# Kernel optimization log

Hardware: AMD Instinct MI355X
Metric: run time of the kernel (lower is better)

Reference implementation:

```python
import jax, jax.numpy as jnp
import numpy as np

N_NODES = 100000
N_EDGES = 400000
N_GRAPHS = 4096
D = 300          # emb_dim
L = 5            # num_layers
NUM_ATOM, NUM_CHIR = 120, 3
NUM_BOND, NUM_DIR = 6, 3
SELF_LOOP_BOND = 4
TEMP = 0.04


def setup_inputs() -> dict:
    key = jax.random.key(0)
    ks = jax.random.split(key, 24)
    inp = {}
    # graph batch 0
    inp["x0"] = jax.random.randint(ks[0], (N_NODES, 2), 0, 3)
    inp["edge_index0"] = jax.random.randint(ks[1], (2, N_EDGES), 0, N_NODES)
    inp["edge_attr0"] = jax.random.randint(ks[2], (N_EDGES, 2), 0, 3)
    inp["batch_ids0"] = jnp.sort(jax.random.randint(ks[3], (N_NODES,), 0, N_GRAPHS))
    inp["dangling0"] = jax.random.randint(ks[4], (N_GRAPHS,), 0, N_NODES)
    # graph batch 1
    inp["x1"] = jax.random.randint(ks[5], (N_NODES, 2), 0, 3)
    inp["edge_index1"] = jax.random.randint(ks[6], (2, N_EDGES), 0, N_NODES)
    inp["edge_attr1"] = jax.random.randint(ks[7], (N_EDGES, 2), 0, 3)
    inp["batch_ids1"] = jnp.sort(jax.random.randint(ks[8], (N_NODES,), 0, N_GRAPHS))
    inp["dangling1"] = jax.random.randint(ks[9], (N_GRAPHS,), 0, N_NODES)
    # shared encoder parameters
    g = lambda i, shp, s=0.1: (jax.random.normal(ks[i], shp, jnp.float32) * s)
    inp["atom_emb1"] = g(10, (NUM_ATOM, D))
    inp["atom_emb2"] = g(11, (NUM_CHIR, D))
    inp["eemb1"] = g(12, (L, NUM_BOND, D))
    inp["eemb2"] = g(13, (L, NUM_DIR, D))
    inp["W1"] = g(14, (L, D, 2 * D))
    inp["b1"] = jnp.zeros((L, 2 * D), jnp.float32)
    inp["W2"] = g(15, (L, 2 * D, D))
    inp["b2"] = jnp.zeros((L, D), jnp.float32)
    inp["bn_g"] = jnp.ones((L, D), jnp.float32)
    inp["bn_b"] = jnp.zeros((L, D), jnp.float32)
    # projectors stacked: 0=projector0, 1=projector1, 2=dangling_proj0, 3=dangling_proj1
    inp["pW1"] = g(16, (4, D, D))
    inp["pb1"] = jnp.zeros((4, D), jnp.float32)
    inp["pW2"] = g(17, (4, D, D))
    inp["pb2"] = jnp.zeros((4, D), jnp.float32)
    return inp


def _encode(x, edge_index, edge_attr, atom_emb1, atom_emb2,
            eemb1, eemb2, W1, b1, W2, b2, bn_g, bn_b):
    # initial node embedding: sum of atom-type and chirality embeddings
    h = atom_emb1[x[:, 0]] + atom_emb2[x[:, 1]]          # [N, D]
    src, dst = edge_index[0], edge_index[1]
    for l in range(L):
        e = eemb1[l][edge_attr[:, 0]] + eemb2[l][edge_attr[:, 1]]  # [E, D]
        msg = h[src] + e                                           # [E, D]
        agg = jax.ops.segment_sum(msg, dst, num_segments=h.shape[0])
        # self-loop with bond type 4, direction 0 (pretrain-gnns GINConv)
        agg = agg + h + eemb1[l][SELF_LOOP_BOND] + eemb2[l][0]
        z = jax.nn.relu(agg @ W1[l] + b1[l]) @ W2[l] + b2[l]       # GIN MLP
        mu = jnp.mean(z, axis=0)
        var = jnp.var(z, axis=0)
        z = (z - mu) * jax.lax.rsqrt(var + 1e-5) * bn_g[l] + bn_b[l]
        h = z if l == L - 1 else jax.nn.relu(z)                    # no ReLU on last layer
    return h


def _mlp(x, w1, bb1, w2, bb2):
    return jax.nn.relu(x @ w1 + bb1) @ w2 + bb2


def _branch(h, batch_ids, dangling, proj_i, dproj_i, pW1, pb1, pW2, pb2):
    pooled = jax.ops.segment_sum(h, batch_ids, num_segments=N_GRAPHS)
    counts = jax.ops.segment_sum(jnp.ones((h.shape[0],), h.dtype), batch_ids,
                                 num_segments=N_GRAPHS)
    pooled = pooled / jnp.maximum(counts, 1.0)[:, None]            # global_mean_pool
    out = _mlp(pooled, pW1[proj_i], pb1[proj_i], pW2[proj_i], pb2[proj_i])
    out = out + _mlp(h[dangling], pW1[dproj_i], pb1[dproj_i], pW2[dproj_i], pb2[dproj_i])
    return out / jnp.linalg.norm(out, axis=1, keepdims=True)       # L2 normalize


def reference(x0, edge_index0, edge_attr0, batch_ids0, dangling0,
              x1, edge_index1, edge_attr1, batch_ids1, dangling1,
              atom_emb1, atom_emb2, eemb1, eemb2, W1, b1, W2, b2, bn_g, bn_b,
              pW1, pb1, pW2, pb2):
    h0 = _encode(x0, edge_index0, edge_attr0, atom_emb1, atom_emb2,
                 eemb1, eemb2, W1, b1, W2, b2, bn_g, bn_b)
    f0 = _branch(h0, batch_ids0, dangling0, 0, 2, pW1, pb1, pW2, pb2)
    h1 = _encode(x1, edge_index1, edge_attr1, atom_emb1, atom_emb2,
                 eemb1, eemb2, W1, b1, W2, b2, bn_g, bn_b)
    f1 = _branch(h1, batch_ids1, dangling1, 1, 3, pW1, pb1, pW2, pb2)
    logits = (f0 @ f1.T) / TEMP                                    # [G, G]
    return logits
```

## Files before the change

### kernel.cpp

```cpp
#include <hip/hip_runtime.h>

#define NN    100000
#define NE    400000
#define NG    4096
#define LL    5
#define MPAD  100096
#define NCHUNK 98

typedef unsigned short u16;
typedef __attribute__((ext_vector_type(8))) _Float16 half8;
typedef __attribute__((ext_vector_type(4))) _Float16 hv4;
typedef __attribute__((ext_vector_type(4))) float float4v;
typedef __attribute__((ext_vector_type(16))) float float16v;

__device__ __forceinline__ float b2f(u16 u){
  union { float f; unsigned u; } c; c.u = ((unsigned)u)<<16; return c.f;
}
__device__ __forceinline__ u16 f2b(float f){
  union { float f; unsigned u; } c; c.f = f;
  unsigned x = c.u;
  return (u16)((x + 0x7fffu + ((x>>16)&1u)) >> 16);
}
__device__ __forceinline__ float h2f(u16 u){
  union { u16 s; _Float16 h; } c; c.s = u; return (float)c.h;
}
__device__ __forceinline__ u16 f2h(float f){
  union { u16 s; _Float16 h; } c; c.h = (_Float16)f; return c.s;
}
__device__ __forceinline__ void g2l16(const u16* g, u16* l){
  __builtin_amdgcn_global_load_lds((const __attribute__((address_space(1))) void*)g,
                                   (__attribute__((address_space(3))) void*)l, 16, 0, 0);
}

__global__ __launch_bounds__(256) void detect_dtype(const u16* __restrict__ p, int* __restrict__ flag){
  int i = blockIdx.x*256 + threadIdx.x;
  float v = b2f(p[i]);
  if (!(fabsf(v) <= 1e4f)) atomicOr(flag, 1);
}
__global__ __launch_bounds__(256) void cvt_param(const void* __restrict__ src, u16* __restrict__ dst,
                                                 int n, const int* __restrict__ flag){
  int i = blockIdx.x*256 + threadIdx.x;
  if (i >= n) return;
  float v = (*flag) ? ((const float*)src)[i] : b2f(((const u16*)src)[i]);
  dst[i] = f2h(v);
}

__global__ __launch_bounds__(256) void zero32(unsigned* __restrict__ p, int n){
  int i = blockIdx.x*256 + threadIdx.x;
  if (i < n) p[i] = 0u;
}

__global__ __launch_bounds__(256) void tpad(const u16* __restrict__ src, u16* __restrict__ dst,
                                            int L, int K, int N, int Kp, int Np){
  int idx = blockIdx.x*256 + threadIdx.x;
  if (idx >= L*Np*Kp) return;
  int l = idx/(Np*Kp); int r = idx - l*Np*Kp; int n = r/Kp; int k = r - n*Kp;
  dst[idx] = (n<N && k<K) ? src[(l*K + k)*N + n] : (u16)0;
}

__global__ __launch_bounds__(256) void ecomb_build(const u16* __restrict__ ee1, const u16* __restrict__ ee2,
                                                   u16* __restrict__ ec){
  int idx = blockIdx.x*256 + threadIdx.x;
  if (idx >= LL*18*160) return;
  int l = idx/(18*160); int r = idx - l*18*160; int c = r/160; int p = r - c*160;
  int a0 = c/3, a1 = c - a0*3;
  u16 o0=0,o1=0;
  if (p < 150){
    int d = 2*p;
    o0 = f2h(h2f(ee1[(l*6+a0)*300+d  ]) + h2f(ee2[(l*3+a1)*300+d  ]));
    o1 = f2h(h2f(ee1[(l*6+a0)*300+d+1]) + h2f(ee2[(l*3+a1)*300+d+1]));
  }
  ((ushort2*)ec)[idx] = make_ushort2(o0,o1);
}

__global__ __launch_bounds__(256) void node_init(const int* __restrict__ x, const u16* __restrict__ ae1,
                                                 const u16* __restrict__ ae2, u16* __restrict__ h){
  int idx = blockIdx.x*256 + threadIdx.x;
  if (idx >= MPAD*160) return;
  int n = idx/160, p = idx - n*160;
  u16 o0=0,o1=0;
  if (n < NN && p < 150){
    int a = x[2*n], ch = x[2*n+1];
    int d = 2*p;
    o0 = f2h(h2f(ae1[a*300+d  ]) + h2f(ae2[ch*300+d  ]));
    o1 = f2h(h2f(ae1[a*300+d+1]) + h2f(ae2[ch*300+d+1]));
  }
  ((ushort2*)h)[idx] = make_ushort2(o0,o1);
}

__global__ __launch_bounds__(256) void hist(const int* __restrict__ ei, int* __restrict__ counts){
  int e = blockIdx.x*256 + threadIdx.x;
  if (e >= NE) return;
  atomicAdd(&counts[ei[NE + e]], 1);
}
__global__ __launch_bounds__(256) void scan_chunks(const int* __restrict__ counts, int* __restrict__ csums){
  __shared__ int sd[256];
  int base = blockIdx.x*1024;
  int s = 0;
  for (int i = threadIdx.x; i < 1024; i += 256){ int g = base+i; if (g < NN) s += counts[g]; }
  sd[threadIdx.x] = s; __syncthreads();
  for (int off=128; off>0; off>>=1){ if (threadIdx.x < off) sd[threadIdx.x] += sd[threadIdx.x+off]; __syncthreads(); }
  if (threadIdx.x == 0) csums[blockIdx.x] = sd[0];
}
__global__ __launch_bounds__(128) void scan_base(const int* __restrict__ csums, int* __restrict__ cbase,
                                                 int* __restrict__ offsets){
  __shared__ int sd[128];
  int tid = threadIdx.x;
  int v = (tid < NCHUNK) ? csums[tid] : 0;
  sd[tid] = v; __syncthreads();
  for (int off=1; off<128; off<<=1){
    int t = (tid >= off) ? sd[tid-off] : 0; __syncthreads();
    sd[tid] += t; __syncthreads();
  }
  if (tid < NCHUNK) cbase[tid] = sd[tid] - v;
  if (tid == 0) offsets[NN] = sd[NCHUNK-1];
}
__global__ __launch_bounds__(256) void scan_final(const int* __restrict__ counts, const int* __restrict__ cbase,
                                                  int* __restrict__ offsets){
  __shared__ int sd[256];
  int tid = threadIdx.x;
  int base = blockIdx.x*1024 + tid*4;
  int v0 = (base   < NN) ? counts[base  ] : 0;
  int v1 = (base+1 < NN) ? counts[base+1] : 0;
  int v2 = (base+2 < NN) ? counts[base+2] : 0;
  int v3 = (base+3 < NN) ? counts[base+3] : 0;
  int s = v0+v1+v2+v3;
  sd[tid] = s; __syncthreads();
  for (int off=1; off<256; off<<=1){
    int t = (tid >= off) ? sd[tid-off] : 0; __syncthreads();
    sd[tid] += t; __syncthreads();
  }
  int run = cbase[blockIdx.x] + sd[tid] - s;
  if (base   < NN){ offsets[base  ] = run; } run += v0;
  if (base+1 < NN){ offsets[base+1] = run; } run += v1;
  if (base+2 < NN){ offsets[base+2] = run; } run += v2;
  if (base+3 < NN){ offsets[base+3] = run; }
}
__global__ __launch_bounds__(256) void fill_perm(const int* __restrict__ ei, const int* __restrict__ ea,
                                                 const int* __restrict__ offsets,
                                                 int* __restrict__ cursor, int* __restrict__ pk){
  int e = blockIdx.x*256 + threadIdx.x;
  if (e >= NE) return;
  int d = ei[NE + e];
  int src = ei[e];
  int c = ea[2*e]*3 + ea[2*e+1];
  int pos = offsets[d] + atomicAdd(&cursor[d], 1);
  pk[pos] = src*32 + c;
}

__global__ __launch_bounds__(256) void aggregate(
    const u16* __restrict__ h, const u16* __restrict__ ecL,
    const int* __restrict__ offsets, const int* __restrict__ pk,
    u16* __restrict__ agg)
{
  __shared__ u16 ecs[18*320];
  for (int i = threadIdx.x; i < 18*160; i += 256)
    ((ushort2*)ecs)[i] = ((const ushort2*)ecL)[i];
  __syncthreads();
  int node = blockIdx.x*4 + (threadIdx.x>>6);
  int lane = threadIdx.x & 63;
  bool tl = lane < 16;
  const hv4* h4 = (const hv4*)h;
  const hv4* e4 = (const hv4*)ecs;
  long base = (long)node*80;
  hv4 acc0, acc1 = (hv4)(_Float16)0;
  acc0 = h4[base + lane] + e4[12*80 + lane];
  if (tl) acc1 = h4[base + 64 + lane] + e4[12*80 + 64 + lane];
  if (node < NN){
    int s = offsets[node], en = offsets[node+1];
    int i = s;
    while (i + 3 < en){
      int p0 = pk[i], p1 = pk[i+1], p2 = pk[i+2], p3 = pk[i+3]; i += 4;
      long b0 = (long)(p0>>5)*80, b1 = (long)(p1>>5)*80;
      long b2 = (long)(p2>>5)*80, b3 = (long)(p3>>5)*80;
      int c0 = (p0&31)*80, c1 = (p1&31)*80, c2 = (p2&31)*80, c3 = (p3&31)*80;
      hv4 a0 = h4[b0+lane], a1 = h4[b1+lane], a2 = h4[b2+lane], a3 = h4[b3+lane];
      hv4 e0 = e4[c0+lane], e1 = e4[c1+lane], e2 = e4[c2+lane], e3 = e4[c3+lane];
      acc0 += (a0+e0); acc0 += (a1+e1); acc0 += (a2+e2); acc0 += (a3+e3);
      if (tl){
        hv4 x0 = h4[b0+64+lane], x1 = h4[b1+64+lane];
        hv4 x2 = h4[b2+64+lane], x3 = h4[b3+64+lane];
        hv4 y0 = e4[c0+64+lane], y1 = e4[c1+64+lane];
        hv4 y2 = e4[c2+64+lane], y3 = e4[c3+64+lane];
        acc1 += (x0+y0); acc1 += (x1+y1); acc1 += (x2+y2); acc1 += (x3+y3);
      }
    }
    while (i < en){
      int p0 = pk[i]; ++i;
      long b0 = (long)(p0>>5)*80; int c0 = (p0&31)*80;
      acc0 += (h4[b0+lane] + e4[c0+lane]);
      if (tl) acc1 += (h4[b0+64+lane] + e4[c0+64+lane]);
    }
  }
  hv4* a4 = (hv4*)agg;
  a4[base + lane] = acc0;
  if (tl) a4[base + 64 + lane] = acc1;
}

__global__ __launch_bounds__(512, 2) void gin_mlp(
    const u16* __restrict__ A,
    const u16* __restrict__ W1Tl,
    const u16* __restrict__ b1l,
    const u16* __restrict__ W2Tl,
    const u16* __restrict__ b2l,
    u16* __restrict__ Z,
    float* __restrict__ colsum, float* __restrict__ colsumsq)
{
  __shared__ __align__(16) u16 lds[32768];
  u16* uS = lds;
  u16* Ws = lds + 8192;
  int tid = threadIdx.x;
  int wave = tid>>6, lane = tid&63;
  int n5 = lane & 31, hi = lane >> 5;
  int q = lane>>4, r = lane&15;
  int rg = wave>>1, ch = wave&1;
  int wr = wave>>2, wc = wave&3;
  int m0 = blockIdx.x*128;

  half8 aReg[20];
  const u16* Arow = A + (long)(m0 + rg*32 + n5)*320 + hi*8;
  #pragma unroll
  for (int kc=0; kc<20; ++kc) aReg[kc] = *(const half8*)(Arow + kc*16);

  float4v zacc[4][6];
  #pragma unroll
  for (int i=0;i<4;i++)
    #pragma unroll
    for (int j=0;j<6;j++) zacc[i][j] = (float4v){0.f,0.f,0.f,0.f};

  for (int t1=0; t1<10; ++t1){
    int n1_0 = t1*64;
    __syncthreads();
    #pragma unroll
    for (int rnd=0; rnd<5; ++rnd){
      int ck = rnd*512 + tid;
      int n = ck/41, k8 = ck - n*41;
      const u16* src = (k8 < 40) ? (W1Tl + (long)(n1_0 + n)*320 + k8*8) : W1Tl;
      g2l16(src, Ws + ck*8);
    }
    if (tid < 64){
      int ck = 2560 + tid;
      int n = ck/41, k8 = ck - n*41;
      const u16* src = (k8 < 40) ? (W1Tl + (long)(n1_0 + n)*320 + k8*8) : W1Tl;
      g2l16(src, Ws + ck*8);
    }
    __syncthreads();
    float16v uacc = (float16v)(0.f);
    #pragma unroll
    for (int kc=0; kc<20; ++kc){
      half8 bw = *(const half8*)&Ws[(ch*32 + n5)*328 + kc*16 + hi*8];
      uacc = __builtin_amdgcn_mfma_f32_32x32x16_f16(aReg[kc], bw, uacc, 0,0,0);
    }
    {
      int n1g = n1_0 + ch*32 + n5;
      float bv = (n1g < 600) ? h2f(b1l[n1g]) : 0.f;
      u16* uw = uS + ch*4096 + n5;
      #pragma unroll
      for (int reg=0; reg<16; ++reg){
        int row = rg*32 + (reg&3) + 8*(reg>>2) + 4*hi;
        float v = fmaxf(uacc[reg] + bv, 0.f);
        uw[row*32] = f2h(v);
      }
    }
    __syncthreads();
    #pragma unroll
    for (int i=0;i<6;i++){
      int idx = tid*8 + i*4096;
      int kc2 = idx / 12288;
      int rem = idx - kc2*12288;
      int n2 = rem >> 5, k8 = rem & 31;
      g2l16(W2Tl + (long)n2*640 + n1_0 + kc2*32 + k8, Ws + idx);
    }
    __syncthreads();
    #pragma unroll
    for (int kc2=0; kc2<2; ++kc2){
      half8 af[4], bf[6];
      #pragma unroll
      for (int i=0;i<4;i++) af[i] = *(const half8*)&uS[kc2*4096 + (wr*64+i*16+r)*32 + q*8];
      #pragma unroll
      for (int j=0;j<6;j++) bf[j] = *(const half8*)&Ws[kc2*12288 + (wc*96+j*16+r)*32 + q*8];
      #pragma unroll
      for (int i=0;i<4;i++)
        #pragma unroll
        for (int j=0;j<6;j++)
          zacc[i][j] = __builtin_amdgcn_mfma_f32_16x16x32_f16(af[i], bf[j], zacc[i][j], 0,0,0);
    }
  }
  #pragma unroll
  for (int j=0;j<6;j++){
    int c = wc*96 + j*16 + r;
    float bv = (c < 300) ? h2f(b2l[c]) : 0.f;
    float s1 = 0.f, s2 = 0.f;
    #pragma unroll
    for (int i=0;i<4;i++){
      int rowb = m0 + wr*64 + i*16 + q*4;
      #pragma unroll
      for (int t=0;t<4;t++){
        float v = zacc[i][j][t] + bv;
        int gr = rowb + t;
        if (c < 320) Z[(long)gr*320 + c] = f2h(v);
        if (gr < NN){ s1 += v; s2 += v*v; }
      }
    }
    s1 += __shfl_xor(s1,16); s1 += __shfl_xor(s1,32);
    s2 += __shfl_xor(s2,16); s2 += __shfl_xor(s2,32);
    if (q == 0 && c < 384){ atomicAdd(&colsum[c], s1); atomicAdd(&colsumsq[c], s2); }
  }
}

__global__ __launch_bounds__(256) void gemm_nt(
    const u16* __restrict__ A, int lda,
    const u16* __restrict__ BT, int ldb,
    int Kp,
    const u16* __restrict__ bias, int Nreal,
    float scale, int dorelu, int omode, int Ncap,
    void* __restrict__ Cv, int ldc,
    const int* __restrict__ outmode)
{
  __shared__ __align__(16) u16 As[128*32];
  __shared__ __align__(16) u16 Bs[128*32];
  int tid = threadIdx.x;
  int wave = tid>>6, lane = tid&63;
  int wr = (wave>>1)&1, wc = wave&1;
  int m0 = blockIdx.x*128, n0 = blockIdx.y*128;
  int q = lane>>4, r = lane&15;
  int srow = tid>>2, scol = (tid&3)*8;
  const u16* Ag0 = A  + (long)(m0+srow)*lda + scol;
  const u16* Ag1 = A  + (long)(m0+64+srow)*lda + scol;
  const u16* Bg0 = BT + (long)(n0+srow)*ldb + scol;
  const u16* Bg1 = BT + (long)(n0+64+srow)*ldb + scol;
  u16* Asl0 = &As[tid*8];
  u16* Asl1 = &As[64*32 + tid*8];
  u16* Bsl0 = &Bs[tid*8];
  u16* Bsl1 = &Bs[64*32 + tid*8];
  float4v acc[4][4];
  #pragma unroll
  for (int i=0;i<4;i++)
    #pragma unroll
    for (int j=0;j<4;j++) acc[i][j] = (float4v){0.f,0.f,0.f,0.f};

  for (int k0=0; k0<Kp; k0+=32){
    g2l16(Ag0+k0, Asl0);
    g2l16(Ag1+k0, Asl1);
    g2l16(Bg0+k0, Bsl0);
    g2l16(Bg1+k0, Bsl1);
    __syncthreads();
    half8 af[4], bf[4];
    #pragma unroll
    for (int i=0;i<4;i++) af[i] = *(const half8*)&As[(wr*64+i*16+r)*32 + q*8];
    #pragma unroll
    for (int j=0;j<4;j++) bf[j] = *(const half8*)&Bs[(wc*64+j*16+r)*32 + q*8];
    #pragma unroll
    for (int i=0;i<4;i++)
      #pragma unroll
      for (int j=0;j<4;j++)
        acc[i][j] = __builtin_amdgcn_mfma_f32_16x16x32_f16(af[i], bf[j], acc[i][j], 0,0,0);
    __syncthreads();
  }

  int ob = omode;
  if (outmode) ob = (*outmode) ? 0 : 1;
  u16* Ch = (u16*)Cv; float* Cf = (float*)Cv;
  #pragma unroll
  for (int j=0;j<4;j++){
    int c = n0 + wc*64 + j*16 + r;
    float bv = (bias && c < Nreal) ? h2f(bias[c]) : 0.f;
    #pragma unroll
    for (int i=0;i<4;i++){
      int rowb = m0 + wr*64 + i*16 + q*4;
      #pragma unroll
      for (int tt=0; tt<4; ++tt){
        float v = acc[i][j][tt] + bv;
        if (dorelu) v = fmaxf(v, 0.f);
        v *= scale;
        int gr = rowb + tt;
        if (c < Ncap){
          long o = (long)gr*ldc + c;
          if (ob == 2)      Ch[o] = f2h(v);
          else if (ob == 1) Ch[o] = f2b(v);
          else              Cf[o] = v;
        }
      }
    }
  }
}

__global__ __launch_bounds__(320) void bn_finalize(const float* __restrict__ st, const u16* __restrict__ g,
                                                   const u16* __restrict__ b, float* __restrict__ sc,
                                                   float* __restrict__ sh){
  int c = threadIdx.x;
  if (c >= 300) return;
  float mu  = st[c] * (1.0f/NN);
  float var = st[384+c] * (1.0f/NN) - mu*mu;
  float inv = rsqrtf(var + 1e-5f);
  float gg = h2f(g[c]) * inv;
  sc[c] = gg; sh[c] = h2f(b[c]) - mu*gg;
}
__global__ __launch_bounds__(256) void bn_apply(const u16* __restrict__ z, const float* __restrict__ sc,
                                                const float* __restrict__ sh, u16* __restrict__ h, int dorelu){
  int idx = blockIdx.x*256 + threadIdx.x;
  if (idx >= NN*150) return;
  int n = idx/150, p = idx - n*150;
  ushort2 zz = ((const ushort2*)z)[n*160 + p];
  int d = 2*p;
  float v0 = h2f(zz.x)*sc[d  ] + sh[d  ];
  float v1 = h2f(zz.y)*sc[d+1] + sh[d+1];
  if (dorelu){ v0 = fmaxf(v0,0.f); v1 = fmaxf(v1,0.f); }
  ((ushort2*)h)[n*160 + p] = make_ushort2(f2h(v0), f2h(v1));
}

__global__ __launch_bounds__(256) void graph_starts(const int* __restrict__ ids, int* __restrict__ starts){
  int i = blockIdx.x*256 + threadIdx.x;
  if (i >= NN) return;
  int b = ids[i];
  if (i == 0){ for (int g=0; g<=b; ++g) starts[g] = 0; }
  else { int p = ids[i-1]; for (int g=p+1; g<=b; ++g) starts[g] = i; }
  if (i == NN-1){ for (int g=b+1; g<=NG; ++g) starts[g] = NN; }
}
__global__ __launch_bounds__(256) void pool_kernel(const u16* __restrict__ h, const int* __restrict__ starts,
                                                   u16* __restrict__ pooled){
  int g = blockIdx.x*4 + (threadIdx.x>>6);
  int lane = threadIdx.x & 63;
  if (g >= NG) return;
  int s = starts[g], e = starts[g+1];
  int cnt = e - s; if (cnt < 1) cnt = 1;
  float inv = 1.0f/(float)cnt;
  float ax[3] = {0,0,0}, ay[3] = {0,0,0};
  const ushort2* h2 = (const ushort2*)h;
  for (int row=s; row<e; ++row){
    long base = (long)row*160;
    #pragma unroll
    for (int jp=0; jp<3; ++jp){
      int p = jp*64 + lane;
      if (p < 160){ ushort2 v = h2[base+p]; ax[jp] += h2f(v.x); ay[jp] += h2f(v.y); }
    }
  }
  ushort2* o2 = (ushort2*)pooled;
  #pragma unroll
  for (int jp=0; jp<3; ++jp){
    int p = jp*64 + lane;
    if (p < 160) o2[g*160+p] = make_ushort2(f2h(ax[jp]*inv), f2h(ay[jp]*inv));
  }
}
__global__ __launch_bounds__(256) void gather_rows(const u16* __restrict__ h, const int* __restrict__ idxs,
                                                   u16* __restrict__ out){
  int idx = blockIdx.x*256 + threadIdx.x;
  if (idx >= NG*160) return;
  int g = idx/160, p = idx - g*160;
  ((ushort2*)out)[idx] = ((const ushort2*)h)[(long)idxs[g]*160 + p];
}
__global__ __launch_bounds__(256) void add_norm(const float* __restrict__ vp, const float* __restrict__ vd,
                                                u16* __restrict__ f){
  int g = blockIdx.x*4 + (threadIdx.x>>6);
  int lane = threadIdx.x & 63;
  if (g >= NG) return;
  float vals[5]; float ss = 0.f;
  #pragma unroll
  for (int t=0; t<5; ++t){
    int d = lane + 64*t; float v = 0.f;
    if (d < 300) v = vp[g*320+d] + vd[g*320+d];
    vals[t] = v; ss += v*v;
  }
  #pragma unroll
  for (int off=32; off>0; off>>=1) ss += __shfl_xor(ss, off);
  float inv = rsqrtf(ss);
  #pragma unroll
  for (int t=0; t<5; ++t){
    int d = lane + 64*t;
    if (d < 320) f[g*320+d] = f2h(d < 300 ? vals[t]*inv : 0.f);
  }
}

extern "C" void kernel_launch(void* const* d_in, const int* in_sizes, int n_in,
                              void* d_out, int out_size, void* d_ws, size_t ws_size,
                              hipStream_t stream)
{
  const int* xin[2]  = {(const int*)d_in[0], (const int*)d_in[5]};
  const int* ei[2]   = {(const int*)d_in[1], (const int*)d_in[6]};
  const int* ea[2]   = {(const int*)d_in[2], (const int*)d_in[7]};
  const int* bid[2]  = {(const int*)d_in[3], (const int*)d_in[8]};
  const int* dang[2] = {(const int*)d_in[4], (const int*)d_in[9]};
  (void)in_sizes; (void)n_in; (void)out_size; (void)ws_size;

  char* w = (char*)d_ws;
  auto alloc = [&](size_t bytes)->char* {
    char* p = w; w += (bytes + 255) & ~(size_t)255; return p;
  };
  u16* hA   = (u16*)alloc((size_t)MPAD*320*2);
  u16* agg  = (u16*)alloc((size_t)MPAD*320*2);
  u16* z    = agg;
  u16*   pooled = (u16*)alloc((size_t)NG*320*2);
  u16*   hd     = (u16*)alloc((size_t)NG*320*2);
  u16*   ubuf   = (u16*)alloc((size_t)NG*384*2);
  float* vpb    = (float*)alloc((size_t)NG*320*4);
  float* vdb    = (float*)alloc((size_t)NG*320*4);
  u16* ec   = (u16*)alloc((size_t)LL*18*320*2);
  u16* W1T  = (u16*)alloc((size_t)LL*640*320*2);
  u16* W2T  = (u16*)alloc((size_t)LL*384*640*2);
  u16* pW1T = (u16*)alloc((size_t)4*384*320*2);
  u16* pW2T = (u16*)alloc((size_t)4*384*384*2);
  int* counts = (int*)alloc((size_t)NN*4);
  int* cursor = (int*)alloc((size_t)NN*4);
  int* offs   = (int*)alloc((size_t)(NN+1)*4);
  int* perm   = (int*)alloc((size_t)NE*4);
  int* csums  = (int*)alloc(512);
  int* cbase  = (int*)alloc(512);
  float* stats = (float*)alloc(768*4);
  float* bnsc  = (float*)alloc(384*4);
  float* bnsh  = (float*)alloc(384*4);
  int* starts  = (int*)alloc((size_t)(NG+1)*4);
  u16* f0b     = (u16*)alloc((size_t)NG*320*2);
  u16* f1b     = (u16*)alloc((size_t)NG*320*2);
  int* dflag   = (int*)alloc(256);
  const int pcnt[14] = {36000, 900, 9000, 4500, 900000, 3000, 900000, 1500,
                        1500, 1500, 360000, 1200, 360000, 1200};
  u16* parena = (u16*)alloc((size_t)2580300*2 + 14*256);
  u16* pp[14];
  { size_t off = 0;
    for (int i=0;i<14;i++){ pp[i] = parena + off; off += (size_t)((pcnt[i]+127)&~127); } }
  u16* ae1 = pp[0];  u16* ae2 = pp[1];  u16* ee1 = pp[2];  u16* ee2 = pp[3];
  u16* W1  = pp[4];  u16* b1  = pp[5];  u16* W2  = pp[6];  u16* b2  = pp[7];
  u16* bng = pp[8];  u16* bnb = pp[9];  u16* pW1 = pp[10]; u16* pb1 = pp[11];
  u16* pW2 = pp[12]; u16* pb2 = pp[13];

  auto cdiv = [](long a, long b){ return (int)((a + b - 1)/b); };
  auto gemm = [&](const u16* A, int lda, const u16* BT, int ldb, int Kp,
                  const u16* bias, int Nreal, float scale, int relu, int omode, int Ncap,
                  void* C, int ldc, int gx, int gy, const int* om){
    gemm_nt<<<dim3(gx,gy), 256, 0, stream>>>(A,lda,BT,ldb,Kp,bias,Nreal,scale,relu,omode,Ncap,
                                             C,ldc,om);
  };

  zero32<<<1,256,0,stream>>>((unsigned*)dflag, 1);
  detect_dtype<<<16,256,0,stream>>>((const u16*)d_in[14], dflag);
  for (int i=0;i<14;i++)
    cvt_param<<<cdiv(pcnt[i],256),256,0,stream>>>(d_in[10+i], pp[i], pcnt[i], dflag);

  tpad<<<cdiv((long)LL*640*320,256),256,0,stream>>>(W1,  W1T,  LL, 300, 600, 320, 640);
  tpad<<<cdiv((long)LL*384*640,256),256,0,stream>>>(W2,  W2T,  LL, 600, 300, 640, 384);
  tpad<<<cdiv((long)4*384*320,256),256,0,stream>>>(pW1, pW1T, 4,  300, 300, 320, 384);
  tpad<<<cdiv((long)4*384*384,256),256,0,stream>>>(pW2, pW2T, 4,  300, 300, 384, 384);
  ecomb_build<<<cdiv((long)LL*18*160,256),256,0,stream>>>(ee1, ee2, ec);

  for (int br=0; br<2; ++br){
    u16* fo = br ? f1b : f0b;
    node_init<<<cdiv((long)MPAD*160,256),256,0,stream>>>(xin[br], ae1, ae2, hA);
    zero32<<<cdiv(NN,256),256,0,stream>>>((unsigned*)counts, NN);
    hist<<<cdiv(NE,256),256,0,stream>>>(ei[br], counts);
    scan_chunks<<<NCHUNK,256,0,stream>>>(counts, csums);
    scan_base<<<1,128,0,stream>>>(csums, cbase, offs);
    scan_final<<<NCHUNK,256,0,stream>>>(counts, cbase, offs);
    zero32<<<cdiv(NN,256),256,0,stream>>>((unsigned*)cursor, NN);
    fill_perm<<<cdiv(NE,256),256,0,stream>>>(ei[br], ea[br], offs, cursor, perm);

    for (int l=0; l<LL; ++l){
      aggregate<<<MPAD/4,256,0,stream>>>(hA, ec + (size_t)l*18*320, offs, perm, agg);
      zero32<<<3,256,0,stream>>>((unsigned*)stats, 768);
      gin_mlp<<<MPAD/128, 512, 0, stream>>>(agg,
          W1T + (size_t)l*640*320, b1 + l*600,
          W2T + (size_t)l*384*640, b2 + l*300,
          z, stats, stats+384);
      bn_finalize<<<1,320,0,stream>>>(stats, bng + l*300, bnb + l*300, bnsc, bnsh);
      bn_apply<<<cdiv((long)NN*150,256),256,0,stream>>>(z, bnsc, bnsh, hA, (l < LL-1) ? 1 : 0);
    }

    graph_starts<<<cdiv(NN,256),256,0,stream>>>(bid[br], starts);
    pool_kernel<<<NG/4,256,0,stream>>>(hA, starts, pooled);
    gather_rows<<<cdiv((long)NG*160,256),256,0,stream>>>(hA, dang[br], hd);

    int pi = br, dpi = 2 + br;
    gemm(pooled, 320, pW1T + (size_t)pi*384*320, 320, 320,
         pb1 + pi*300, 300, 1.f, 1, 2, 384, ubuf, 384, NG/128, 3, nullptr);
    gemm(ubuf, 384, pW2T + (size_t)pi*384*384, 384, 384,
         pb2 + pi*300, 300, 1.f, 0, 0, 320, vpb, 320, NG/128, 3, nullptr);
    gemm(hd, 320, pW1T + (size_t)dpi*384*320, 320, 320,
         pb1 + dpi*300, 300, 1.f, 1, 2, 384, ubuf, 384, NG/128, 3, nullptr);
    gemm(ubuf, 384, pW2T + (size_t)dpi*384*384, 384, 384,
         pb2 + dpi*300, 300, 1.f, 0, 0, 320, vdb, 320, NG/128, 3, nullptr);
    add_norm<<<NG/4,256,0,stream>>>(vpb, vdb, fo);
  }

  gemm(f0b, 320, f1b, 320, 320, nullptr, 0, 25.0f, 0, 1, NG,
       d_out, NG, NG/128, NG/128, dflag);
}
```

Before: 3.695 ms.

## Triple-buffer gemm_nt loads, remap tiles per XCD, vectorize bn_apply, nontemporal stores

The gemm_nt kernel now keeps three LDS stages, issuing asynchronous global-to-LDS loads two K-steps ahead with explicit vmcnt waits. This replaces the two __syncthreads per iteration with a single barrier. Workgroup ids are remapped so that neighbouring tiles land on the same XCD, and the projector gemm grids are transposed to match the new m/n mapping. bn_apply now processes 8 halves per thread with 16-byte loads and writes zeros into the padding columns. The aggregate and gin_mlp outputs are written with nontemporal stores. These changes target latency in the small GEMMs and memory efficiency in the elementwise passes; the cost is more LDS per gemm block and a risk of slower reloads of agg and z if they would otherwise stay in cache.

```diff
diff --git a/kernel.cpp b/kernel.cpp
--- a/kernel.cpp
+++ b/kernel.cpp
@@ -12,6 +12,7 @@
 typedef __attribute__((ext_vector_type(4))) _Float16 hv4;
 typedef __attribute__((ext_vector_type(4))) float float4v;
 typedef __attribute__((ext_vector_type(16))) float float16v;
+typedef __attribute__((ext_vector_type(8))) short short8v;
 
 __device__ __forceinline__ float b2f(u16 u){
   union { float f; unsigned u; } c; c.u = ((unsigned)u)<<16; return c.f;
@@ -193,8 +194,8 @@
     }
   }
   hv4* a4 = (hv4*)agg;
-  a4[base + lane] = acc0;
-  if (tl) a4[base + 64 + lane] = acc1;
+  __builtin_nontemporal_store(acc0, &a4[base + lane]);
+  if (tl) __builtin_nontemporal_store(acc1, &a4[base + 64 + lane]);
 }
 
 __global__ __launch_bounds__(512, 2) void gin_mlp(
@@ -298,7 +299,7 @@
       for (int t=0;t<4;t++){
         float v = zacc[i][j][t] + bv;
         int gr = rowb + t;
-        if (c < 320) Z[(long)gr*320 + c] = f2h(v);
+        if (c < 320) __builtin_nontemporal_store(f2h(v), &Z[(long)gr*320 + c]);
         if (gr < NN){ s1 += v; s2 += v*v; }
       }
     }
@@ -317,45 +318,59 @@
     void* __restrict__ Cv, int ldc,
     const int* __restrict__ outmode)
 {
-  __shared__ __align__(16) u16 As[128*32];
-  __shared__ __align__(16) u16 Bs[128*32];
+  __shared__ __align__(16) u16 As[3][128*32];
+  __shared__ __align__(16) u16 Bs[3][128*32];
   int tid = threadIdx.x;
   int wave = tid>>6, lane = tid&63;
   int wr = (wave>>1)&1, wc = wave&1;
-  int m0 = blockIdx.x*128, n0 = blockIdx.y*128;
+  int nwg  = gridDim.x*gridDim.y;
+  int flat = blockIdx.y*gridDim.x + blockIdx.x;
+  int qd = nwg>>3, rm = nwg&7;
+  int xcd = flat&7, sub = flat>>3;
+  int wgid = (xcd<rm ? xcd*(qd+1) : rm*(qd+1)+(xcd-rm)*qd) + sub;
+  int nt = wgid % gridDim.x, mt = wgid / gridDim.x;
+  int m0 = mt*128, n0 = nt*128;
   int q = lane>>4, r = lane&15;
   int srow = tid>>2, scol = (tid&3)*8;
   const u16* Ag0 = A  + (long)(m0+srow)*lda + scol;
   const u16* Ag1 = A  + (long)(m0+64+srow)*lda + scol;
   const u16* Bg0 = BT + (long)(n0+srow)*ldb + scol;
   const u16* Bg1 = BT + (long)(n0+64+srow)*ldb + scol;
-  u16* Asl0 = &As[tid*8];
-  u16* Asl1 = &As[64*32 + tid*8];
-  u16* Bsl0 = &Bs[tid*8];
-  u16* Bsl1 = &Bs[64*32 + tid*8];
   float4v acc[4][4];
   #pragma unroll
   for (int i=0;i<4;i++)
     #pragma unroll
     for (int j=0;j<4;j++) acc[i][j] = (float4v){0.f,0.f,0.f,0.f};
 
-  for (int k0=0; k0<Kp; k0+=32){
-    g2l16(Ag0+k0, Asl0);
-    g2l16(Ag1+k0, Asl1);
-    g2l16(Bg0+k0, Bsl0);
-    g2l16(Bg1+k0, Bsl1);
-    __syncthreads();
+  int nk = Kp >> 5;
+  {
+    g2l16(Ag0, &As[0][tid*8]);     g2l16(Ag1, &As[0][2048+tid*8]);
+    g2l16(Bg0, &Bs[0][tid*8]);     g2l16(Bg1, &Bs[0][2048+tid*8]);
+    if (nk > 1){
+      g2l16(Ag0+32, &As[1][tid*8]);  g2l16(Ag1+32, &As[1][2048+tid*8]);
+      g2l16(Bg0+32, &Bs[1][tid*8]);  g2l16(Bg1+32, &Bs[1][2048+tid*8]);
+    }
+  }
+  for (int t=0; t<nk; ++t){
+    int cur = t % 3;
+    if (t+1 < nk) asm volatile("s_waitcnt vmcnt(4)" ::: "memory");
+    else          asm volatile("s_waitcnt vmcnt(0)" ::: "memory");
+    __builtin_amdgcn_s_barrier();
+    if (t+2 < nk){
+      int b = (t+2)%3, k0 = (t+2)*32;
+      g2l16(Ag0+k0, &As[b][tid*8]);  g2l16(Ag1+k0, &As[b][2048+tid*8]);
+      g2l16(Bg0+k0, &Bs[b][tid*8]);  g2l16(Bg1+k0, &Bs[b][2048+tid*8]);
+    }
     half8 af[4], bf[4];
     #pragma unroll
-    for (int i=0;i<4;i++) af[i] = *(const half8*)&As[(wr*64+i*16+r)*32 + q*8];
-    #pragma unroll
-    for (int j=0;j<4;j++) bf[j] = *(const half8*)&Bs[(wc*64+j*16+r)*32 + q*8];
+    for (int i=0;i<4;i++) af[i] = *(const half8*)&As[cur][(wr*64+i*16+r)*32 + q*8];
+    #pragma unroll
+    for (int j=0;j<4;j++) bf[j] = *(const half8*)&Bs[cur][(wc*64+j*16+r)*32 + q*8];
     #pragma unroll
     for (int i=0;i<4;i++)
       #pragma unroll
       for (int j=0;j<4;j++)
         acc[i][j] = __builtin_amdgcn_mfma_f32_16x16x32_f16(af[i], bf[j], acc[i][j], 0,0,0);
-    __syncthreads();
   }
 
   int ob = omode;
@@ -399,14 +414,19 @@
 __global__ __launch_bounds__(256) void bn_apply(const u16* __restrict__ z, const float* __restrict__ sc,
                                                 const float* __restrict__ sh, u16* __restrict__ h, int dorelu){
   int idx = blockIdx.x*256 + threadIdx.x;
-  if (idx >= NN*150) return;
-  int n = idx/150, p = idx - n*150;
-  ushort2 zz = ((const ushort2*)z)[n*160 + p];
-  int d = 2*p;
-  float v0 = h2f(zz.x)*sc[d  ] + sh[d  ];
-  float v1 = h2f(zz.y)*sc[d+1] + sh[d+1];
-  if (dorelu){ v0 = fmaxf(v0,0.f); v1 = fmaxf(v1,0.f); }
-  ((ushort2*)h)[n*160 + p] = make_ushort2(f2h(v0), f2h(v1));
+  if (idx >= NN*40) return;
+  int n = idx/40, p = idx - n*40;
+  short8v zz = ((const short8v*)z)[(long)n*40 + p];
+  short8v out;
+  #pragma unroll
+  for (int e=0; e<8; ++e){
+    int d = p*8 + e;
+    float v = h2f((u16)zz[e])*sc[d] + sh[d];
+    if (dorelu) v = fmaxf(v, 0.f);
+    out[e] = (short)f2h(v);
+    if (d >= 300) out[e] = 0;
+  }
+  ((short8v*)h)[(long)n*40 + p] = out;
 }
 
 __global__ __launch_bounds__(256) void graph_starts(const int* __restrict__ ids, int* __restrict__ starts){
@@ -561,7 +581,7 @@
           W2T + (size_t)l*384*640, b2 + l*300,
           z, stats, stats+384);
       bn_finalize<<<1,320,0,stream>>>(stats, bng + l*300, bnb + l*300, bnsc, bnsh);
-      bn_apply<<<cdiv((long)NN*150,256),256,0,stream>>>(z, bnsc, bnsh, hA, (l < LL-1) ? 1 : 0);
+      bn_apply<<<cdiv((long)NN*40,256),256,0,stream>>>(z, bnsc, bnsh, hA, (l < LL-1) ? 1 : 0);
     }
 
     graph_starts<<<cdiv(NN,256),256,0,stream>>>(bid[br], starts);
@@ -570,13 +590,13 @@
 
     int pi = br, dpi = 2 + br;
     gemm(pooled, 320, pW1T + (size_t)pi*384*320, 320, 320,
-         pb1 + pi*300, 300, 1.f, 1, 2, 384, ubuf, 384, NG/128, 3, nullptr);
+         pb1 + pi*300, 300, 1.f, 1, 2, 384, ubuf, 384, 3, NG/128, nullptr);
     gemm(ubuf, 384, pW2T + (size_t)pi*384*384, 384, 384,
-         pb2 + pi*300, 300, 1.f, 0, 0, 320, vpb, 320, NG/128, 3, nullptr);
+         pb2 + pi*300, 300, 1.f, 0, 0, 320, vpb, 320, 3, NG/128, nullptr);
     gemm(hd, 320, pW1T + (size_t)dpi*384*320, 320, 320,
-         pb1 + dpi*300, 300, 1.f, 1, 2, 384, ubuf, 384, NG/128, 3, nullptr);
+         pb1 + dpi*300, 300, 1.f, 1, 2, 384, ubuf, 384, 3, NG/128, nullptr);
     gemm(ubuf, 384, pW2T + (size_t)dpi*384*384, 384, 384,
-         pb2 + dpi*300, 300, 1.f, 0, 0, 320, vdb, 320, NG/128, 3, nullptr);
+         pb2 + dpi*300, 300, 1.f, 0, 0, 320, vdb, 320, 3, NG/128, nullptr);
     add_norm<<<NG/4,256,0,stream>>>(vpb, vdb, fo);
   }
 
```

New measurement: 3.547 ms (median of 2 runs). 4.0% less time.
